# Kernel optimization log

Measured on AMD Instinct MI355X. Metric: run time of the kernel, lower is better.

The kernel has to match this reference:

```python
import jax, jax.numpy as jnp
import numpy as np

BATCH = 8192
FEAT_DIM = 768
MULTIPLE_CONVEX = 4
NUM_CONVEX = BATCH * MULTIPLE_CONVEX
NUM_LABELS = 150
UNSEEN_LABEL_ID = 150


def setup_inputs() -> dict:
    key = jax.random.key(0)
    k_z, k_s = jax.random.split(key)
    z = jax.random.normal(k_z, (BATCH, FEAT_DIM), dtype=jnp.float32)
    s = jax.random.uniform(k_s, (NUM_CONVEX,), dtype=jnp.float32)

    # Host-side rejection sampling of index pairs with distinct labels,
    # mirroring the original np.random.choice-until-labels-differ loop.
    rng = np.random.default_rng(0)
    labels = rng.integers(0, NUM_LABELS, size=BATCH)
    idx_i = rng.integers(0, BATCH, size=NUM_CONVEX)
    idx_j = rng.integers(0, BATCH, size=NUM_CONVEX)
    bad = labels[idx_i] == labels[idx_j]
    while bad.any():
        idx_j[bad] = rng.integers(0, BATCH, size=int(bad.sum()))
        bad = labels[idx_i] == labels[idx_j]

    return {
        "z": z,
        "label_ids": jnp.asarray(labels, dtype=jnp.int64 if jax.config.jax_enable_x64 else jnp.int32),
        "idx_i": jnp.asarray(idx_i, dtype=jnp.int32),
        "idx_j": jnp.asarray(idx_j, dtype=jnp.int32),
        "s": s,
    }


def reference(z, label_ids, idx_i, idx_j, s):
    # convex[k] = s[k] * z[i_k] + (1 - s[k]) * z[j_k]  -- gather + axpy
    sw = s[:, None]  # [NUM_CONVEX, 1]
    convex = sw * z[idx_i] + (1.0 - sw) * z[idx_j]  # [NUM_CONVEX, FEAT_DIM]
    z_out = jnp.concatenate([z, convex], axis=0)  # [BATCH+NUM_CONVEX, FEAT_DIM]
    unseen = jnp.full((idx_i.shape[0],), UNSEEN_LABEL_ID, dtype=label_ids.dtype)
    labels_out = jnp.concatenate([label_ids, unseen], axis=0)
    return z_out, labels_out
```

## Files before the change

### kernel.cpp

```cpp
#include <hip/hip_runtime.h>
#include <stdint.h>

#define BATCH 8192
#define FEAT 768
#define NCVX 32768
#define NOUT (BATCH + NCVX)
#define UNSEEN 150

#define ROW_CHUNKS (FEAT / 4)
constexpr int COPY_CHUNKS = BATCH * ROW_CHUNKS;
constexpr int CVX_CHUNKS  = NCVX  * ROW_CHUNKS;
constexpr int LAB_CHUNKS  = NOUT / 4;
constexpr int TOTAL_CHUNKS = COPY_CHUNKS + CVX_CHUNKS + LAB_CHUNKS;

__global__ __launch_bounds__(256) void ConvexSampler_39006892982339_kernel(
    const float* __restrict__ z,
    const int*   __restrict__ labels,
    const int*   __restrict__ idx_i,
    const int*   __restrict__ idx_j,
    const float* __restrict__ s,
    float*       __restrict__ out)
{
    int t = blockIdx.x * 256 + threadIdx.x;
    if (t >= TOTAL_CHUNKS) return;

    if (t < COPY_CHUNKS) {
        ((float4*)out)[t] = ((const float4*)z)[t];
    } else if (t < COPY_CHUNKS + CVX_CHUNKS) {
        int c   = t - COPY_CHUNKS;
        int row = c / ROW_CHUNKS;
        int col = c - row * ROW_CHUNKS;
        float sw  = s[row];
        float sw1 = 1.0f - sw;
        const float4* ap = (const float4*)(z + (size_t)idx_i[row] * FEAT) + col;
        const float4* bp = (const float4*)(z + (size_t)idx_j[row] * FEAT) + col;
        float4 a = *ap;
        float4 b = *bp;
        float4 r;
        r.x = sw * a.x + sw1 * b.x;
        r.y = sw * a.y + sw1 * b.y;
        r.z = sw * a.z + sw1 * b.z;
        r.w = sw * a.w + sw1 * b.w;
        ((float4*)out)[t] = r;
    } else {
        int c    = t - (COPY_CHUNKS + CVX_CHUNKS);
        int base = c * 4;
        float4 r;
        r.x = (float)(base + 0 < BATCH ? labels[base + 0] : UNSEEN);
        r.y = (float)(base + 1 < BATCH ? labels[base + 1] : UNSEEN);
        r.z = (float)(base + 2 < BATCH ? labels[base + 2] : UNSEEN);
        r.w = (float)(base + 3 < BATCH ? labels[base + 3] : UNSEEN);
        ((float4*)(out + (size_t)NOUT * FEAT))[c] = r;
    }
}

extern "C" void kernel_launch(void* const* d_in, const int* in_sizes, int n_in,
                              void* d_out, int out_size, void* d_ws, size_t ws_size,
                              hipStream_t stream) {
    const float* z      = (const float*)d_in[0];
    const int*   labels = (const int*)d_in[1];
    const int*   idx_i  = (const int*)d_in[2];
    const int*   idx_j  = (const int*)d_in[3];
    const float* s      = (const float*)d_in[4];
    float*       out    = (float*)d_out;

    int blocks = (TOTAL_CHUNKS + 255) / 256;
    ConvexSampler_39006892982339_kernel<<<blocks, 256, 0, stream>>>(
        z, labels, idx_i, idx_j, s, out);
}
```

Measured before the change: 169.1 us.

## Map one wavefront per output row with nontemporal stores and batched loads

Restructures the kernel so each 64-lane wavefront handles one whole output row of 768 floats (3 float4 per lane). This removes the per-thread row/col division and the per-element index and scale loads. Each wave issues all six gather loads before computing, which exposes more memory-level parallelism. Stores use nontemporal hints so the large output does not evict the reused z rows from cache. The risk is fewer threads in flight per byte moved, and nontemporal behavior may vary on this hardware.

```diff
diff --git a/kernel.cpp b/kernel.cpp
--- a/kernel.cpp
+++ b/kernel.cpp
@@ -7,11 +7,12 @@
 #define NOUT (BATCH + NCVX)
 #define UNSEEN 150
 
-#define ROW_CHUNKS (FEAT / 4)
-constexpr int COPY_CHUNKS = BATCH * ROW_CHUNKS;
-constexpr int CVX_CHUNKS  = NCVX  * ROW_CHUNKS;
-constexpr int LAB_CHUNKS  = NOUT / 4;
-constexpr int TOTAL_CHUNKS = COPY_CHUNKS + CVX_CHUNKS + LAB_CHUNKS;
+typedef float vf4 __attribute__((ext_vector_type(4)));
+
+constexpr int ROWS_PER_BLOCK = 4;
+constexpr int ROW_BLOCKS = NOUT / ROWS_PER_BLOCK;
+constexpr int LAB_BLOCKS = NOUT / 1024;
+constexpr int TOTAL_BLOCKS = ROW_BLOCKS + LAB_BLOCKS;
 
 __global__ __launch_bounds__(256) void ConvexSampler_39006892982339_kernel(
     const float* __restrict__ z,
@@ -21,36 +22,51 @@
     const float* __restrict__ s,
     float*       __restrict__ out)
 {
-    int t = blockIdx.x * 256 + threadIdx.x;
-    if (t >= TOTAL_CHUNKS) return;
-
-    if (t < COPY_CHUNKS) {
-        ((float4*)out)[t] = ((const float4*)z)[t];
-    } else if (t < COPY_CHUNKS + CVX_CHUNKS) {
-        int c   = t - COPY_CHUNKS;
-        int row = c / ROW_CHUNKS;
-        int col = c - row * ROW_CHUNKS;
-        float sw  = s[row];
-        float sw1 = 1.0f - sw;
-        const float4* ap = (const float4*)(z + (size_t)idx_i[row] * FEAT) + col;
-        const float4* bp = (const float4*)(z + (size_t)idx_j[row] * FEAT) + col;
-        float4 a = *ap;
-        float4 b = *bp;
-        float4 r;
-        r.x = sw * a.x + sw1 * b.x;
-        r.y = sw * a.y + sw1 * b.y;
-        r.z = sw * a.z + sw1 * b.z;
-        r.w = sw * a.w + sw1 * b.w;
-        ((float4*)out)[t] = r;
+    int blk = blockIdx.x;
+    if (blk < ROW_BLOCKS) {
+        int wave = threadIdx.x >> 6;
+        int lane = threadIdx.x & 63;
+        int row  = blk * ROWS_PER_BLOCK + wave;
+        vf4* op = (vf4*)(out + (size_t)row * FEAT);
+        if (row < BATCH) {
+            const vf4* zp = (const vf4*)(z + (size_t)row * FEAT);
+#pragma unroll
+            for (int j = 0; j < 3; ++j) {
+                vf4 v = zp[j * 64 + lane];
+                __builtin_nontemporal_store(v, op + j * 64 + lane);
+            }
+        } else {
+            int c = row - BATCH;
+            float sw  = s[c];
+            float sw1 = 1.0f - sw;
+            const vf4* ap = (const vf4*)(z + (size_t)idx_i[c] * FEAT);
+            const vf4* bp = (const vf4*)(z + (size_t)idx_j[c] * FEAT);
+            vf4 a0 = ap[0 * 64 + lane];
+            vf4 a1 = ap[1 * 64 + lane];
+            vf4 a2 = ap[2 * 64 + lane];
+            vf4 b0 = bp[0 * 64 + lane];
+            vf4 b1 = bp[1 * 64 + lane];
+            vf4 b2 = bp[2 * 64 + lane];
+            vf4 r0 = sw * a0 + sw1 * b0;
+            vf4 r1 = sw * a1 + sw1 * b1;
+            vf4 r2 = sw * a2 + sw1 * b2;
+            __builtin_nontemporal_store(r0, op + 0 * 64 + lane);
+            __builtin_nontemporal_store(r1, op + 1 * 64 + lane);
+            __builtin_nontemporal_store(r2, op + 2 * 64 + lane);
+        }
     } else {
-        int c    = t - (COPY_CHUNKS + CVX_CHUNKS);
-        int base = c * 4;
-        float4 r;
-        r.x = (float)(base + 0 < BATCH ? labels[base + 0] : UNSEEN);
-        r.y = (float)(base + 1 < BATCH ? labels[base + 1] : UNSEEN);
-        r.z = (float)(base + 2 < BATCH ? labels[base + 2] : UNSEEN);
-        r.w = (float)(base + 3 < BATCH ? labels[base + 3] : UNSEEN);
-        ((float4*)(out + (size_t)NOUT * FEAT))[c] = r;
+        int c4   = (blk - ROW_BLOCKS) * 256 + threadIdx.x;
+        int base = c4 * 4;
+        vf4 r;
+        if (base < BATCH) {
+            r.x = (float)labels[base + 0];
+            r.y = (float)labels[base + 1];
+            r.z = (float)labels[base + 2];
+            r.w = (float)labels[base + 3];
+        } else {
+            r = (vf4)((float)UNSEEN);
+        }
+        __builtin_nontemporal_store(r, (vf4*)(out + (size_t)NOUT * FEAT) + c4);
     }
 }
 
@@ -64,7 +80,6 @@
     const float* s      = (const float*)d_in[4];
     float*       out    = (float*)d_out;
 
-    int blocks = (TOTAL_CHUNKS + 255) / 256;
-    ConvexSampler_39006892982339_kernel<<<blocks, 256, 0, stream>>>(
+    ConvexSampler_39006892982339_kernel<<<TOTAL_BLOCKS, 256, 0, stream>>>(
         z, labels, idx_i, idx_j, s, out);
 }
```

Result: slower. 173.7 us (+2.7%).
